# Kernel tuning notes

Hardware: AMD Instinct MI355X
Metric: run time of the kernel (lower is better)

Reference implementation:

```python
import jax, jax.numpy as jnp
import numpy as np

DIM = 768
NUM_HEADS = 12
HEAD_DIM = DIM // NUM_HEADS
SCALE = HEAD_DIM ** -0.5


def setup_inputs() -> dict:
    key = jax.random.key(0)
    k_x, k_qkv, k_pw, k_pb = jax.random.split(key, 4)
    x = jax.random.normal(k_x, (1, 4096, DIM), dtype=jnp.float32)
    # nn.Linear weights stored as [out, in]; apply as x @ W.T
    w_qkv = jax.random.normal(k_qkv, (3 * DIM, DIM), dtype=jnp.float32) * (DIM ** -0.5)
    w_proj = jax.random.normal(k_pw, (DIM, DIM), dtype=jnp.float32) * (DIM ** -0.5)
    b_proj = jax.random.normal(k_pb, (DIM,), dtype=jnp.float32) * 0.01
    return {"x": x, "w_qkv": w_qkv, "w_proj": w_proj, "b_proj": b_proj}


def reference(x, w_qkv, w_proj, b_proj):
    b, s, d = x.shape
    qkv = jnp.einsum('bsd,ed->bse', x, w_qkv)            # [B,S,3D]
    qkv = qkv.reshape(b, s, 3, NUM_HEADS, HEAD_DIM)
    qkv = jnp.transpose(qkv, (2, 0, 3, 1, 4))            # [3,B,H,S,hd]
    q, k, v = qkv[0], qkv[1], qkv[2]
    scores = jnp.einsum('bhqe,bhke->bhqk', q, k) * SCALE  # [B,H,S,S]
    probs = jax.nn.softmax(scores, axis=-1)
    attended = jnp.einsum('bhqk,bhke->bhqe', probs, v)    # [B,H,S,hd]
    attended = jnp.transpose(attended, (0, 2, 1, 3)).reshape(b, s, d)
    return jnp.einsum('bsd,ed->bse', attended, w_proj) + b_proj
```

## Files before the change

kernel.cpp:

```cpp
#include <hip/hip_runtime.h>
#include <hip/hip_bf16.h>

using short8 = __attribute__((ext_vector_type(8))) short;
using s16x4  = __attribute__((ext_vector_type(4))) short;
using f32x4  = __attribute__((ext_vector_type(4))) float;
using f32x16 = __attribute__((ext_vector_type(16))) float;
using v2i    = __attribute__((ext_vector_type(2))) int;

#define DIM   768
#define D3    2304
#define SEQL  4096
#define NHEAD 12
#define NSPLIT 2

#if defined(__has_builtin)
#  if __has_builtin(__builtin_amdgcn_permlane32_swap)
#    define HAVE_PLSWAP 1
#  endif
#endif

static __device__ __forceinline__ short f2bs(float f) {
  union { __hip_bfloat16 h; short s; } u;
  u.h = __float2bfloat16(f);
  return u.s;
}

static __device__ __forceinline__ float bf2f(short s) {
  union { unsigned u; float f; } x;
  x.u = ((unsigned)(unsigned short)s) << 16;
  return x.f;
}

static __device__ __forceinline__ int cvtpk(float lo, float hi) {
  int r;
  asm("v_cvt_pk_bf16_f32 %0, %1, %2" : "=v"(r) : "v"(lo), "v"(hi));
  return r;
}

static __device__ __forceinline__ float ex2(float x) {
  float r;
  asm("v_exp_f32 %0, %1" : "=v"(r) : "v"(x));
  return r;
}

static __device__ __forceinline__ void gl_lds16(const void* g, void* lds) {
  __builtin_amdgcn_global_load_lds((const __attribute__((address_space(1))) void*)g,
                                   (__attribute__((address_space(3))) void*)lds, 16, 0, 0);
}

__global__ __launch_bounds__(256) void cvt3_kernel(const float* __restrict__ x,
                                                   const float* __restrict__ wq,
                                                   const float* __restrict__ wp,
                                                   short* __restrict__ xb,
                                                   short* __restrict__ wqb,
                                                   short* __restrict__ wpb) {
  int b = blockIdx.x;
  const float* src; short* dst; int base; float sc = 1.0f;
  if (b < 3072)      { src = x;  dst = xb;  base = b * 1024; }
  else if (b < 4800) { src = wq; dst = wqb; base = (b - 3072) * 1024;
                       if (base < DIM * DIM) sc = 0.125f * 1.4426950408889634f; }
  else               { src = wp; dst = wpb; base = (b - 4800) * 1024; }
  int i = base + threadIdx.x * 4;
  f32x4 v = *(const f32x4*)(src + i);
  s16x4 o;
  #pragma unroll
  for (int j = 0; j < 4; ++j) o[j] = f2bs(v[j] * sc);
  *(s16x4*)(dst + i) = o;
}

template <bool BF16OUT>
__global__ __launch_bounds__(256) void gemm_bt(const short* __restrict__ A,
                                               const short* __restrict__ B,
                                               short* __restrict__ Cb,
                                               float* __restrict__ Cf,
                                               const float* __restrict__ bias,
                                               int M, int N, int K) {
  __shared__ short As[128 * 64];
  __shared__ short Bs[128 * 64];
  const int tid = threadIdx.x;
  const int l  = tid & 63;
  const int w  = tid >> 6;
  const int g  = l >> 4, lc = l & 15;
  const int wr = w >> 1, wc = w & 1;
  const int m0 = blockIdx.y * 128, n0 = blockIdx.x * 128;
  const int trow = tid >> 3;
  const int tcol = (tid & 7) * 8;
  const int sswz = 8 * (trow & 7);
  const int rswz = 8 * (lc & 7);

  f32x4 acc[4][4];
  #pragma unroll
  for (int a = 0; a < 4; ++a)
    #pragma unroll
    for (int b = 0; b < 4; ++b) acc[a][b] = (f32x4){0.f, 0.f, 0.f, 0.f};

  for (int k0 = 0; k0 < K; k0 += 64) {
    __syncthreads();
    #pragma unroll
    for (int i = 0; i < 4; ++i) {
      int row = i * 32 + trow;
      gl_lds16(A + (size_t)(m0 + row) * K + k0 + (tcol ^ sswz), As + row * 64 + tcol);
      gl_lds16(B + (size_t)(n0 + row) * K + k0 + (tcol ^ sswz), Bs + row * 64 + tcol);
    }
    __syncthreads();
    #pragma unroll
    for (int kk = 0; kk < 2; ++kk) {
      short8 af[4], bf[4];
      #pragma unroll
      for (int mt = 0; mt < 4; ++mt)
        af[mt] = *(const short8*)(As + (wr * 64 + mt * 16 + lc) * 64 + ((kk * 32 + g * 8) ^ rswz));
      #pragma unroll
      for (int nt = 0; nt < 4; ++nt)
        bf[nt] = *(const short8*)(Bs + (wc * 64 + nt * 16 + lc) * 64 + ((kk * 32 + g * 8) ^ rswz));
      #pragma unroll
      for (int mt = 0; mt < 4; ++mt)
        #pragma unroll
        for (int nt = 0; nt < 4; ++nt)
          acc[mt][nt] = __builtin_amdgcn_mfma_f32_16x16x32_bf16(af[mt], bf[nt], acc[mt][nt], 0, 0, 0);
    }
  }

  #pragma unroll
  for (int mt = 0; mt < 4; ++mt)
    #pragma unroll
    for (int nt = 0; nt < 4; ++nt)
      #pragma unroll
      for (int r = 0; r < 4; ++r) {
        int row = m0 + wr * 64 + mt * 16 + g * 4 + r;
        int col = n0 + wc * 64 + nt * 16 + lc;
        float v = acc[mt][nt][r];
        if (BF16OUT) Cb[(size_t)row * N + col] = f2bs(v);
        else         Cf[(size_t)row * N + col] = v + bias[col];
      }
}

template <bool BF16OUT>
__global__ __launch_bounds__(256) void gemm_bt64(const short* __restrict__ A,
                                                 const short* __restrict__ B,
                                                 short* __restrict__ Cb,
                                                 float* __restrict__ Cf,
                                                 const float* __restrict__ bias,
                                                 int M, int N, int K) {
  __shared__ short As[64 * 64];
  __shared__ short Bs[64 * 64];
  const int tid = threadIdx.x;
  const int l  = tid & 63;
  const int w  = tid >> 6;
  const int g  = l >> 4, lc = l & 15;
  const int wr = w >> 1, wc = w & 1;
  const int m0 = blockIdx.y * 64, n0 = blockIdx.x * 64;
  const int rswz = 8 * (lc & 7);

  f32x4 acc[2][2];
  #pragma unroll
  for (int a = 0; a < 2; ++a)
    #pragma unroll
    for (int b = 0; b < 2; ++b) acc[a][b] = (f32x4){0.f, 0.f, 0.f, 0.f};

  for (int k0 = 0; k0 < K; k0 += 64) {
    __syncthreads();
    #pragma unroll
    for (int i = 0; i < 2; ++i) {
      int seg = i * 256 + tid;
      int row = seg >> 3, c = (seg & 7) * 8;
      int swz = 8 * (row & 7);
      gl_lds16(A + (size_t)(m0 + row) * K + k0 + (c ^ swz), As + seg * 8);
      gl_lds16(B + (size_t)(n0 + row) * K + k0 + (c ^ swz), Bs + seg * 8);
    }
    __syncthreads();
    #pragma unroll
    for (int kk = 0; kk < 2; ++kk) {
      short8 af[2], bf[2];
      #pragma unroll
      for (int mt = 0; mt < 2; ++mt)
        af[mt] = *(const short8*)(As + (wr * 32 + mt * 16 + lc) * 64 + ((kk * 32 + g * 8) ^ rswz));
      #pragma unroll
      for (int nt = 0; nt < 2; ++nt)
        bf[nt] = *(const short8*)(Bs + (wc * 32 + nt * 16 + lc) * 64 + ((kk * 32 + g * 8) ^ rswz));
      #pragma unroll
      for (int mt = 0; mt < 2; ++mt)
        #pragma unroll
        for (int nt = 0; nt < 2; ++nt)
          acc[mt][nt] = __builtin_amdgcn_mfma_f32_16x16x32_bf16(af[mt], bf[nt], acc[mt][nt], 0, 0, 0);
    }
  }

  #pragma unroll
  for (int mt = 0; mt < 2; ++mt)
    #pragma unroll
    for (int nt = 0; nt < 2; ++nt)
      #pragma unroll
      for (int r = 0; r < 4; ++r) {
        int row = m0 + wr * 32 + mt * 16 + g * 4 + r;
        int col = n0 + wc * 32 + nt * 16 + lc;
        float v = acc[mt][nt][r];
        if (BF16OUT) Cb[(size_t)row * N + col] = f2bs(v);
        else         Cf[(size_t)row * N + col] = v + bias[col];
      }
}

__global__ __launch_bounds__(256) void transpose_v(const short* __restrict__ qkv,
                                                   short* __restrict__ vtg) {
  __shared__ short T[64][72];
  const int jt = blockIdx.x, hd = blockIdx.y, tid = threadIdx.x;
  #pragma unroll
  for (int i = 0; i < 2; ++i) {
    int idx = i * 256 + tid;
    int r = idx >> 3, c = idx & 7;
    *(short8*)&T[r][8 * c] =
        *(const short8*)(qkv + (size_t)(jt * 64 + r) * D3 + 1536 + hd * 64 + 8 * c);
  }
  __syncthreads();
  #pragma unroll
  for (int i = 0; i < 2; ++i) {
    int idx = i * 256 + tid;
    int d = idx >> 3, jc = idx & 7;
    short8 v;
    #pragma unroll
    for (int e = 0; e < 8; ++e) v[e] = T[8 * jc + e][d];
    *(short8*)(vtg + ((size_t)hd * 64 + d) * 4096 + jt * 64 + 8 * jc) = v;
  }
}

__global__ __launch_bounds__(256) void attn_kernel(const short* __restrict__ qkv,
                                                   const short* __restrict__ vtg,
                                                   short* __restrict__ O0,
                                                   short* __restrict__ O1,
                                                   float* __restrict__ Lp,
                                                   int tpb) {
  __shared__ short Ks[3][64 * 64];
  __shared__ short Vt[3][64 * 64];

  const int lin = blockIdx.x;
  const int swz = (lin & 7) * 96 + (lin >> 3);
  const int qt   = swz & 31;
  const int head = (swz >> 5) % NHEAD;
  const int z    = swz / (32 * NHEAD);

  const int tid = threadIdx.x;
  const int l = tid & 63, w = tid >> 6;
  const int h = l >> 5;
  const int q5 = l & 31;
  const int hoff = head * 64;
  const int qbase = qt * 128 + w * 32;
  const int t0 = z * tpb, tend = t0 + tpb;

  short8 qf[4];
  {
    const short* qrow = qkv + (size_t)(qbase + q5) * D3 + hoff;
    #pragma unroll
    for (int ks = 0; ks < 4; ++ks) qf[ks] = *(const short8*)(qrow + ks * 16 + h * 8);
  }

  f32x16 o[2], o_l;
  #pragma unroll
  for (int nt = 0; nt < 2; ++nt)
    #pragma unroll
    for (int r = 0; r < 16; ++r) o[nt][r] = 0.f;
  #pragma unroll
  for (int r = 0; r < 16; ++r) o_l[r] = 0.f;
  const f32x16 zacc = {};
  const short8 ones8 = {(short)0x3F80, (short)0x3F80, (short)0x3F80, (short)0x3F80,
                        (short)0x3F80, (short)0x3F80, (short)0x3F80, (short)0x3F80};

  const int swzK = 8 * (q5 & 7);

  const int srow = tid >> 3, scol = (tid & 7) * 8;
  const int sswz = 8 * (srow & 7);
  const short* kptr = qkv + (size_t)(t0 * 64 + srow) * D3 + hoff + 768 + (scol ^ sswz);
  const short* vptr = vtg + ((size_t)hoff + srow) * 4096 + t0 * 64 + (scol ^ sswz);

  #define STAGE(BUF)                                                             \
    {                                                                            \
      gl_lds16(kptr,             &Ks[BUF][tid * 8]);                             \
      gl_lds16(kptr + 32 * D3,   &Ks[BUF][(tid + 256) * 8]);                     \
      gl_lds16(vptr,             &Vt[BUF][tid * 8]);                             \
      gl_lds16(vptr + 32 * 4096, &Vt[BUF][(tid + 256) * 8]);                     \
      kptr += 64 * D3;                                                           \
      vptr += 64;                                                                \
    }

  STAGE(0);
  STAGE(1);

  int cur = 0, sb = 2;
  for (int tt = t0; tt < tend; ++tt) {
    if (tt + 1 < tend) asm volatile("s_waitcnt vmcnt(4)" ::: "memory");
    else               asm volatile("s_waitcnt vmcnt(0)" ::: "memory");
    __builtin_amdgcn_s_barrier();
    if (tt + 2 < tend) STAGE(sb);

    f32x16 p[2];
    __builtin_amdgcn_s_setprio(1);
    #pragma unroll
    for (int ks = 0; ks < 4; ++ks) {
      #pragma unroll
      for (int mt = 0; mt < 2; ++mt) {
        short8 kf = *(const short8*)(&Ks[cur][(mt * 32 + q5) * 64
                                              + ((ks * 16 + h * 8) ^ swzK)]);
        p[mt] = __builtin_amdgcn_mfma_f32_32x32x16_bf16(kf, qf[ks],
                                                        ks == 0 ? zacc : p[mt], 0, 0, 0);
      }
    }
    __builtin_amdgcn_s_setprio(0);

    #pragma unroll
    for (int mt = 0; mt < 2; ++mt)
      #pragma unroll
      for (int i = 0; i < 16; ++i) p[mt][i] = ex2(p[mt][i]);

    int D[16];
    #pragma unroll
    for (int mt = 0; mt < 2; ++mt)
      #pragma unroll
      for (int c = 0; c < 4; ++c) {
        D[mt * 8 + c * 2 + 0] = cvtpk(p[mt][4 * c + 0], p[mt][4 * c + 1]);
        D[mt * 8 + c * 2 + 1] = cvtpk(p[mt][4 * c + 2], p[mt][4 * c + 3]);
      }

    __builtin_amdgcn_s_setprio(1);
    #pragma unroll
    for (int ks = 0; ks < 4; ++ks) {
      union { int i[4]; short8 s; } pa;
#ifdef HAVE_PLSWAP
      v2i r02 = __builtin_amdgcn_permlane32_swap(D[4 * ks + 0], D[4 * ks + 2], false, false);
      v2i r13 = __builtin_amdgcn_permlane32_swap(D[4 * ks + 1], D[4 * ks + 3], false, false);
      pa.i[0] = r02[0];
      pa.i[1] = r13[0];
      pa.i[2] = r02[1];
      pa.i[3] = r13[1];
#else
      const bool hh = (h != 0);
      const int a0 = D[4 * ks + 0], a1 = D[4 * ks + 1];
      const int b0 = D[4 * ks + 2], b1 = D[4 * ks + 3];
      int snd0 = hh ? a0 : b0, snd1 = hh ? a1 : b1;
      int r0 = __shfl_xor(snd0, 32), r1 = __shfl_xor(snd1, 32);
      pa.i[0] = hh ? r0 : a0;
      pa.i[1] = hh ? r1 : a1;
      pa.i[2] = hh ? b0 : r0;
      pa.i[3] = hh ? b1 : r1;
#endif
      o_l = __builtin_amdgcn_mfma_f32_32x32x16_bf16(pa.s, ones8, o_l, 0, 0, 0);
      #pragma unroll
      for (int nt = 0; nt < 2; ++nt) {
        short8 vf = *(const short8*)(&Vt[cur][(nt * 32 + q5) * 64
                                              + ((ks * 16 + h * 8) ^ swzK)]);
        o[nt] = __builtin_amdgcn_mfma_f32_32x32x16_bf16(pa.s, vf, o[nt], 0, 0, 0);
      }
    }
    __builtin_amdgcn_s_setprio(0);

    cur = (cur == 2) ? 0 : cur + 1;
    sb  = (sb == 2) ? 0 : sb + 1;
  }

  if (q5 == 0) {
    #pragma unroll
    for (int pp = 0; pp < 4; ++pp)
      #pragma unroll
      for (int r = 0; r < 4; ++r)
        Lp[(size_t)z * SEQL * NHEAD + (qbase + r + 8 * pp + 4 * h) * NHEAD + head] = o_l[4 * pp + r];
  }
  short* Ob = (z == 0) ? O0 : O1;
  #pragma unroll
  for (int nt = 0; nt < 2; ++nt)
    #pragma unroll
    for (int pp = 0; pp < 4; ++pp)
      #pragma unroll
      for (int r = 0; r < 4; ++r) {
        int q = qbase + r + 8 * pp + 4 * h;
        int d = hoff + nt * 32 + q5;
        Ob[(size_t)q * DIM + d] = f2bs(o[nt][4 * pp + r]);
      }
}

__global__ __launch_bounds__(256) void combine_kernel(short* __restrict__ O0,
                                                      const short* __restrict__ O1,
                                                      const float* __restrict__ Lp) {
  int idx = blockIdx.x * 256 + threadIdx.x;
  int e0 = idx * 8;
  if (e0 >= SEQL * DIM) return;
  int q = e0 / DIM, col = e0 % DIM, head = col >> 6;
  float lv = Lp[q * NHEAD + head] + Lp[SEQL * NHEAD + q * NHEAD + head];
  float inv = 1.0f / lv;
  short8 a = *(const short8*)(O0 + e0);
  short8 b = *(const short8*)(O1 + e0);
  short8 r;
  #pragma unroll
  for (int j = 0; j < 8; ++j) r[j] = f2bs((bf2f(a[j]) + bf2f(b[j])) * inv);
  *(short8*)(O0 + e0) = r;
}

extern "C" void kernel_launch(void* const* d_in, const int* in_sizes, int n_in,
                              void* d_out, int out_size, void* d_ws, size_t ws_size,
                              hipStream_t stream) {
  (void)in_sizes; (void)n_in; (void)out_size; (void)ws_size;
  const float* x      = (const float*)d_in[0];
  const float* w_qkv  = (const float*)d_in[1];
  const float* w_proj = (const float*)d_in[2];
  const float* b_proj = (const float*)d_in[3];
  float* out = (float*)d_out;

  short* xb   = (short*)d_ws;
  short* wqb  = xb  + (size_t)SEQL * DIM;
  short* wpb  = wqb + (size_t)D3 * DIM;
  short* qkvb = wpb + (size_t)DIM * DIM;
  short* attb = qkvb + (size_t)SEQL * D3;
  short* Opart1 = xb;
  float* Lpart  = (float*)wqb;
  short* vtg    = (short*)d_out;

  cvt3_kernel<<<5376, 256, 0, stream>>>(x, w_qkv, w_proj, xb, wqb, wpb);
  gemm_bt<true ><<<dim3(D3 / 128, SEQL / 128), 256, 0, stream>>>(xb, wqb, qkvb, nullptr, nullptr, SEQL, D3, DIM);
  transpose_v<<<dim3(SEQL / 64, NHEAD), 256, 0, stream>>>(qkvb, vtg);
  attn_kernel<<<dim3(32 * NHEAD * NSPLIT, 1, 1), 256, 0, stream>>>(qkvb, vtg, attb, Opart1, Lpart,
                                                                   (SEQL / 64) / NSPLIT);
  combine_kernel<<<SEQL * DIM / 8 / 256, 256, 0, stream>>>(attb, Opart1, Lpart);
  gemm_bt64<false><<<dim3(DIM / 64, SEQL / 64), 256, 0, stream>>>(attb, wpb, nullptr, out, b_proj, SEQL, DIM, DIM);
}
```

Baseline: 126.2 us.

## Split attention KV range three ways and double-buffer V to cut LDS

Raises the split-KV factor from two to three, so the attention grid grows from 768 to 1152 blocks with uneven 21/21/22 tile ranges. The combine kernel now sums three partial outputs and normalizers. V staging drops from triple to double buffering while K stays triple buffered, which lowers LDS use per block and may allow more resident blocks. The cost is an extra partial buffer written and read in combine, and V loads get less prefetch slack.

```diff
diff --git a/kernel.cpp b/kernel.cpp
--- a/kernel.cpp
+++ b/kernel.cpp
@@ -11,7 +11,7 @@
 #define D3    2304
 #define SEQL  4096
 #define NHEAD 12
-#define NSPLIT 2
+#define NSPLIT 3
 
 #if defined(__has_builtin)
 #  if __has_builtin(__builtin_amdgcn_permlane32_swap)
@@ -226,13 +226,13 @@
                                                    const short* __restrict__ vtg,
                                                    short* __restrict__ O0,
                                                    short* __restrict__ O1,
-                                                   float* __restrict__ Lp,
-                                                   int tpb) {
+                                                   short* __restrict__ O2,
+                                                   float* __restrict__ Lp) {
   __shared__ short Ks[3][64 * 64];
-  __shared__ short Vt[3][64 * 64];
+  __shared__ short Vt[2][64 * 64];
 
   const int lin = blockIdx.x;
-  const int swz = (lin & 7) * 96 + (lin >> 3);
+  const int swz = (lin & 7) * 144 + (lin >> 3);
   const int qt   = swz & 31;
   const int head = (swz >> 5) % NHEAD;
   const int z    = swz / (32 * NHEAD);
@@ -243,7 +243,7 @@
   const int q5 = l & 31;
   const int hoff = head * 64;
   const int qbase = qt * 128 + w * 32;
-  const int t0 = z * tpb, tend = t0 + tpb;
+  const int t0 = (z * 64) / 3, tend = ((z + 1) * 64) / 3;
 
   short8 qf[4];
   {
@@ -270,25 +270,31 @@
   const short* kptr = qkv + (size_t)(t0 * 64 + srow) * D3 + hoff + 768 + (scol ^ sswz);
   const short* vptr = vtg + ((size_t)hoff + srow) * 4096 + t0 * 64 + (scol ^ sswz);
 
-  #define STAGE(BUF)                                                             \
+  #define STAGE_V(BUF)                                                           \
+    {                                                                            \
+      gl_lds16(vptr,             &Vt[BUF][tid * 8]);                             \
+      gl_lds16(vptr + 32 * 4096, &Vt[BUF][(tid + 256) * 8]);                     \
+      vptr += 64;                                                                \
+    }
+  #define STAGE_K(BUF)                                                           \
     {                                                                            \
       gl_lds16(kptr,             &Ks[BUF][tid * 8]);                             \
       gl_lds16(kptr + 32 * D3,   &Ks[BUF][(tid + 256) * 8]);                     \
-      gl_lds16(vptr,             &Vt[BUF][tid * 8]);                             \
-      gl_lds16(vptr + 32 * 4096, &Vt[BUF][(tid + 256) * 8]);                     \
       kptr += 64 * D3;                                                           \
-      vptr += 64;                                                                \
-    }
-
-  STAGE(0);
-  STAGE(1);
-
-  int cur = 0, sb = 2;
+    }
+
+  STAGE_V(0);
+  STAGE_K(0);
+  STAGE_K(1);
+
+  int kcur = 0, ksb = 2;
   for (int tt = t0; tt < tend; ++tt) {
-    if (tt + 1 < tend) asm volatile("s_waitcnt vmcnt(4)" ::: "memory");
+    const int vcur = (tt - t0) & 1;
+    if (tt + 1 < tend) asm volatile("s_waitcnt vmcnt(2)" ::: "memory");
     else               asm volatile("s_waitcnt vmcnt(0)" ::: "memory");
     __builtin_amdgcn_s_barrier();
-    if (tt + 2 < tend) STAGE(sb);
+    if (tt + 1 < tend) STAGE_V(vcur ^ 1);
+    if (tt + 2 < tend) STAGE_K(ksb);
 
     f32x16 p[2];
     __builtin_amdgcn_s_setprio(1);
@@ -296,8 +302,8 @@
     for (int ks = 0; ks < 4; ++ks) {
       #pragma unroll
       for (int mt = 0; mt < 2; ++mt) {
-        short8 kf = *(const short8*)(&Ks[cur][(mt * 32 + q5) * 64
-                                              + ((ks * 16 + h * 8) ^ swzK)]);
+        short8 kf = *(const short8*)(&Ks[kcur][(mt * 32 + q5) * 64
+                                               + ((ks * 16 + h * 8) ^ swzK)]);
         p[mt] = __builtin_amdgcn_mfma_f32_32x32x16_bf16(kf, qf[ks],
                                                         ks == 0 ? zacc : p[mt], 0, 0, 0);
       }
@@ -343,15 +349,15 @@
       o_l = __builtin_amdgcn_mfma_f32_32x32x16_bf16(pa.s, ones8, o_l, 0, 0, 0);
       #pragma unroll
       for (int nt = 0; nt < 2; ++nt) {
-        short8 vf = *(const short8*)(&Vt[cur][(nt * 32 + q5) * 64
-                                              + ((ks * 16 + h * 8) ^ swzK)]);
+        short8 vf = *(const short8*)(&Vt[vcur][(nt * 32 + q5) * 64
+                                               + ((ks * 16 + h * 8) ^ swzK)]);
         o[nt] = __builtin_amdgcn_mfma_f32_32x32x16_bf16(pa.s, vf, o[nt], 0, 0, 0);
       }
     }
     __builtin_amdgcn_s_setprio(0);
 
-    cur = (cur == 2) ? 0 : cur + 1;
-    sb  = (sb == 2) ? 0 : sb + 1;
+    kcur = (kcur == 2) ? 0 : kcur + 1;
+    ksb  = (ksb == 2) ? 0 : ksb + 1;
   }
 
   if (q5 == 0) {
@@ -361,7 +367,7 @@
       for (int r = 0; r < 4; ++r)
         Lp[(size_t)z * SEQL * NHEAD + (qbase + r + 8 * pp + 4 * h) * NHEAD + head] = o_l[4 * pp + r];
   }
-  short* Ob = (z == 0) ? O0 : O1;
+  short* Ob = (z == 0) ? O0 : (z == 1) ? O1 : O2;
   #pragma unroll
   for (int nt = 0; nt < 2; ++nt)
     #pragma unroll
@@ -376,18 +382,22 @@
 
 __global__ __launch_bounds__(256) void combine_kernel(short* __restrict__ O0,
                                                       const short* __restrict__ O1,
+                                                      const short* __restrict__ O2,
                                                       const float* __restrict__ Lp) {
   int idx = blockIdx.x * 256 + threadIdx.x;
   int e0 = idx * 8;
   if (e0 >= SEQL * DIM) return;
   int q = e0 / DIM, col = e0 % DIM, head = col >> 6;
-  float lv = Lp[q * NHEAD + head] + Lp[SEQL * NHEAD + q * NHEAD + head];
+  int i0 = q * NHEAD + head;
+  float lv = Lp[i0] + Lp[SEQL * NHEAD + i0] + Lp[2 * SEQL * NHEAD + i0];
   float inv = 1.0f / lv;
   short8 a = *(const short8*)(O0 + e0);
   short8 b = *(const short8*)(O1 + e0);
+  short8 c = *(const short8*)(O2 + e0);
   short8 r;
   #pragma unroll
-  for (int j = 0; j < 8; ++j) r[j] = f2bs((bf2f(a[j]) + bf2f(b[j])) * inv);
+  for (int j = 0; j < 8; ++j)
+    r[j] = f2bs((bf2f(a[j]) + bf2f(b[j]) + bf2f(c[j])) * inv);
   *(short8*)(O0 + e0) = r;
 }
 
@@ -409,12 +419,12 @@
   short* Opart1 = xb;
   float* Lpart  = (float*)wqb;
   short* vtg    = (short*)d_out;
+  short* Opart2 = vtg + (size_t)SEQL * DIM;
 
   cvt3_kernel<<<5376, 256, 0, stream>>>(x, w_qkv, w_proj, xb, wqb, wpb);
   gemm_bt<true ><<<dim3(D3 / 128, SEQL / 128), 256, 0, stream>>>(xb, wqb, qkvb, nullptr, nullptr, SEQL, D3, DIM);
   transpose_v<<<dim3(SEQL / 64, NHEAD), 256, 0, stream>>>(qkvb, vtg);
-  attn_kernel<<<dim3(32 * NHEAD * NSPLIT, 1, 1), 256, 0, stream>>>(qkvb, vtg, attb, Opart1, Lpart,
-                                                                   (SEQL / 64) / NSPLIT);
-  combine_kernel<<<SEQL * DIM / 8 / 256, 256, 0, stream>>>(attb, Opart1, Lpart);
+  attn_kernel<<<dim3(32 * NHEAD * NSPLIT, 1, 1), 256, 0, stream>>>(qkvb, vtg, attb, Opart1, Opart2, Lpart);
+  combine_kernel<<<SEQL * DIM / 8 / 256, 256, 0, stream>>>(attb, Opart1, Opart2, Lpart);
   gemm_bt64<false><<<dim3(DIM / 64, SEQL / 64), 256, 0, stream>>>(attb, wpb, nullptr, out, b_proj, SEQL, DIM, DIM);
 }
```

Result: slower. 133.3 us (+5.7%).

## Double-buffer LDS tiles in both GEMM kernels to overlap loads with MFMA

Applied to the files above, without the earlier changes.

Both bf16 GEMM kernels now keep two shared-memory stages and issue direct global-to-LDS loads two K-steps ahead. Explicit vmcnt waits let the next tile's loads stay in flight while MFMAs run on the current one. The goal is to hide global-load latency that the single-buffer load/sync/compute loop left exposed. LDS use doubles, which can lower occupancy, and correctness now depends on the hand-counted vmcnt thresholds matching the number of outstanding loads per stage.

```diff
diff --git a/kernel.cpp b/kernel.cpp
--- a/kernel.cpp
+++ b/kernel.cpp
@@ -75,8 +75,8 @@
                                                float* __restrict__ Cf,
                                                const float* __restrict__ bias,
                                                int M, int N, int K) {
-  __shared__ short As[128 * 64];
-  __shared__ short Bs[128 * 64];
+  __shared__ short As[2][128 * 64];
+  __shared__ short Bs[2][128 * 64];
   const int tid = threadIdx.x;
   const int l  = tid & 63;
   const int w  = tid >> 6;
@@ -94,30 +94,48 @@
     #pragma unroll
     for (int b = 0; b < 4; ++b) acc[a][b] = (f32x4){0.f, 0.f, 0.f, 0.f};
 
-  for (int k0 = 0; k0 < K; k0 += 64) {
-    __syncthreads();
-    #pragma unroll
-    for (int i = 0; i < 4; ++i) {
-      int row = i * 32 + trow;
-      gl_lds16(A + (size_t)(m0 + row) * K + k0 + (tcol ^ sswz), As + row * 64 + tcol);
-      gl_lds16(B + (size_t)(n0 + row) * K + k0 + (tcol ^ sswz), Bs + row * 64 + tcol);
-    }
-    __syncthreads();
+  #define GSTAGE(T, BUF)                                                         \
+    {                                                                            \
+      const int kk0_ = (T) * 64;                                                 \
+      _Pragma("unroll")                                                          \
+      for (int i_ = 0; i_ < 4; ++i_) {                                           \
+        int row_ = i_ * 32 + trow;                                               \
+        gl_lds16(A + (size_t)(m0 + row_) * K + kk0_ + (tcol ^ sswz),             \
+                 As[BUF] + row_ * 64 + tcol);                                    \
+        gl_lds16(B + (size_t)(n0 + row_) * K + kk0_ + (tcol ^ sswz),             \
+                 Bs[BUF] + row_ * 64 + tcol);                                    \
+      }                                                                          \
+    }
+
+  const int T = K / 64;
+  GSTAGE(0, 0);
+  GSTAGE(1, 1);
+
+  for (int t = 0; t < T; ++t) {
+    const int buf = t & 1;
+    if (t + 1 < T) asm volatile("s_waitcnt vmcnt(8)" ::: "memory");
+    else           asm volatile("s_waitcnt vmcnt(0)" ::: "memory");
+    __builtin_amdgcn_s_barrier();
+
     #pragma unroll
     for (int kk = 0; kk < 2; ++kk) {
       short8 af[4], bf[4];
       #pragma unroll
       for (int mt = 0; mt < 4; ++mt)
-        af[mt] = *(const short8*)(As + (wr * 64 + mt * 16 + lc) * 64 + ((kk * 32 + g * 8) ^ rswz));
+        af[mt] = *(const short8*)(As[buf] + (wr * 64 + mt * 16 + lc) * 64 + ((kk * 32 + g * 8) ^ rswz));
       #pragma unroll
       for (int nt = 0; nt < 4; ++nt)
-        bf[nt] = *(const short8*)(Bs + (wc * 64 + nt * 16 + lc) * 64 + ((kk * 32 + g * 8) ^ rswz));
+        bf[nt] = *(const short8*)(Bs[buf] + (wc * 64 + nt * 16 + lc) * 64 + ((kk * 32 + g * 8) ^ rswz));
       #pragma unroll
       for (int mt = 0; mt < 4; ++mt)
         #pragma unroll
         for (int nt = 0; nt < 4; ++nt)
           acc[mt][nt] = __builtin_amdgcn_mfma_f32_16x16x32_bf16(af[mt], bf[nt], acc[mt][nt], 0, 0, 0);
     }
+
+    asm volatile("s_waitcnt lgkmcnt(0)" ::: "memory");
+    __builtin_amdgcn_s_barrier();
+    if (t + 2 < T) GSTAGE(t + 2, buf);
   }
 
   #pragma unroll
@@ -141,8 +159,8 @@
                                                  float* __restrict__ Cf,
                                                  const float* __restrict__ bias,
                                                  int M, int N, int K) {
-  __shared__ short As[64 * 64];
-  __shared__ short Bs[64 * 64];
+  __shared__ short As[2][64 * 64];
+  __shared__ short Bs[2][64 * 64];
   const int tid = threadIdx.x;
   const int l  = tid & 63;
   const int w  = tid >> 6;
@@ -157,32 +175,48 @@
     #pragma unroll
     for (int b = 0; b < 2; ++b) acc[a][b] = (f32x4){0.f, 0.f, 0.f, 0.f};
 
-  for (int k0 = 0; k0 < K; k0 += 64) {
-    __syncthreads();
-    #pragma unroll
-    for (int i = 0; i < 2; ++i) {
-      int seg = i * 256 + tid;
-      int row = seg >> 3, c = (seg & 7) * 8;
-      int swz = 8 * (row & 7);
-      gl_lds16(A + (size_t)(m0 + row) * K + k0 + (c ^ swz), As + seg * 8);
-      gl_lds16(B + (size_t)(n0 + row) * K + k0 + (c ^ swz), Bs + seg * 8);
-    }
-    __syncthreads();
+  #define G64STAGE(T, BUF)                                                       \
+    {                                                                            \
+      const int kk0_ = (T) * 64;                                                 \
+      _Pragma("unroll")                                                          \
+      for (int i_ = 0; i_ < 2; ++i_) {                                           \
+        int seg_ = i_ * 256 + tid;                                               \
+        int row_ = seg_ >> 3, c_ = (seg_ & 7) * 8;                               \
+        int swz_ = 8 * (row_ & 7);                                               \
+        gl_lds16(A + (size_t)(m0 + row_) * K + kk0_ + (c_ ^ swz_), As[BUF] + seg_ * 8); \
+        gl_lds16(B + (size_t)(n0 + row_) * K + kk0_ + (c_ ^ swz_), Bs[BUF] + seg_ * 8); \
+      }                                                                          \
+    }
+
+  const int T = K / 64;
+  G64STAGE(0, 0);
+  G64STAGE(1, 1);
+
+  for (int t = 0; t < T; ++t) {
+    const int buf = t & 1;
+    if (t + 1 < T) asm volatile("s_waitcnt vmcnt(4)" ::: "memory");
+    else           asm volatile("s_waitcnt vmcnt(0)" ::: "memory");
+    __builtin_amdgcn_s_barrier();
+
     #pragma unroll
     for (int kk = 0; kk < 2; ++kk) {
       short8 af[2], bf[2];
       #pragma unroll
       for (int mt = 0; mt < 2; ++mt)
-        af[mt] = *(const short8*)(As + (wr * 32 + mt * 16 + lc) * 64 + ((kk * 32 + g * 8) ^ rswz));
+        af[mt] = *(const short8*)(As[buf] + (wr * 32 + mt * 16 + lc) * 64 + ((kk * 32 + g * 8) ^ rswz));
       #pragma unroll
       for (int nt = 0; nt < 2; ++nt)
-        bf[nt] = *(const short8*)(Bs + (wc * 32 + nt * 16 + lc) * 64 + ((kk * 32 + g * 8) ^ rswz));
+        bf[nt] = *(const short8*)(Bs[buf] + (wc * 32 + nt * 16 + lc) * 64 + ((kk * 32 + g * 8) ^ rswz));
       #pragma unroll
       for (int mt = 0; mt < 2; ++mt)
         #pragma unroll
         for (int nt = 0; nt < 2; ++nt)
           acc[mt][nt] = __builtin_amdgcn_mfma_f32_16x16x32_bf16(af[mt], bf[nt], acc[mt][nt], 0, 0, 0);
     }
+
+    asm volatile("s_waitcnt lgkmcnt(0)" ::: "memory");
+    __builtin_amdgcn_s_barrier();
+    if (t + 2 < T) G64STAGE(t + 2, buf);
   }
 
   #pragma unroll
```

Result: slower. 130.6 us (+3.5%).
